# Optimization experiments

Measured on AMD Instinct MI355X. Metric: run time of the kernel, lower is better.

Reference implementation:

```python
import jax, jax.numpy as jnp
import numpy as np

H, Dh, D = 12, 64, 8          # heads, head dim, depth slices
DS = Dh // D                   # per-depth slice dim = 8
EPS = 1e-6
MAW_STRENGTH = 0.15
ALPHA = 1.0 + 10.0 * MAW_STRENGTH  # 2.5


def _min_max_norm(v, eps=1e-12):
    vmin = v.min(axis=-1, keepdims=True)
    vmax = v.max(axis=-1, keepdims=True)
    return (v - vmin) / jnp.maximum(vmax - vmin, eps)


def setup_inputs() -> dict:
    key = jax.random.key(0)
    ks = jax.random.split(key, 8)
    B, L, E = 2, 768, H * Dh
    s = 0.02
    return {
        "hidden_states": jax.random.normal(ks[0], (B, L, E), jnp.float32),
        "attention_mask": jnp.zeros((B, L), jnp.float32),  # additive mask
        "Wq": jax.random.normal(ks[1], (E, E), jnp.float32) * s,
        "bq": jnp.zeros((E,), jnp.float32),
        "Wk": jax.random.normal(ks[2], (E, E), jnp.float32) * s,
        "bk": jnp.zeros((E,), jnp.float32),
        "Wv": jax.random.normal(ks[3], (E, E), jnp.float32) * s,
        "bv": jnp.zeros((E,), jnp.float32),
    }


def reference(hidden_states, attention_mask, Wq, bq, Wk, bk, Wv, bv):
    B, L, E = hidden_states.shape
    # projections -> [B, H, L, Dh]
    q = (hidden_states @ Wq + bq).reshape(B, L, H, Dh).transpose(0, 2, 1, 3)
    k = (hidden_states @ Wk + bk).reshape(B, L, H, Dh).transpose(0, 2, 1, 3)
    v = (hidden_states @ Wv + bv).reshape(B, L, H, Dh).transpose(0, 2, 1, 3)

    # depth-wise expansion: split head dim into D slices of size DS
    qd = q.reshape(B, H, L, D, DS)
    kd = k.reshape(B, H, L, D, DS)
    scores = jnp.einsum("bhqds,bhkds->bhdqk", qd, kd) / jnp.sqrt(jnp.float32(DS))
    # additive mask [B, Lk] -> [B, 1, 1, 1, Lk]
    scores = scores + attention_mask[:, None, None, None, :]
    attn = jax.nn.softmax(scores, axis=-1)  # [B, H, D, Lq, Lk]

    # statistical depth gating (mode='stat')
    var_k = jnp.var(attn, axis=-1, ddof=1).mean(axis=(1, 3))          # [B, D]
    max_k = attn.max(axis=-1).mean(axis=(1, 3))                        # [B, D]
    p = jnp.clip(attn, EPS, None)
    ent = (-p * jnp.log(p)).sum(axis=-1).mean(axis=(1, 3))             # [B, D]
    hhi = (attn * attn).sum(axis=-1).mean(axis=(1, 3))                 # [B, D]

    score = (0.5 * _min_max_norm(var_k) + 0.3 * _min_max_norm(max_k)
             + 0.2 * _min_max_norm(hhi) - 0.4 * _min_max_norm(ent))
    weights = jax.nn.softmax(ALPHA * score, axis=-1)                   # [B, D]

    # depth compression -> [B, H, Lq, Lk]
    attn4 = jnp.einsum("bhdqk,bd->bhqk", attn, weights)
    ctx = jnp.einsum("bhqk,bhkd->bhqd", attn4, v)                      # [B, H, L, Dh]
    ctx = ctx.transpose(0, 2, 1, 3).reshape(B, L, H * Dh)
    return ctx, attn4
```

## Files before the change

kernel.cpp:

```cpp
#include <hip/hip_runtime.h>

#define BATCH 2
#define L_SEQ 768
#define NH 12
#define DH 64
#define ND 8
#define EMB 768
#define RSQRT8 0.35355339059327373f

#define OFF_Q    0
#define OFF_K    1179648
#define OFF_V    2359296
#define OFF_L    3538944
#define OFF_PART 3686400
#define OFF_P2   6045696
#define OFF_W    6046464

__global__ __launch_bounds__(256) void k1_qkv(
    const float* __restrict__ hs,
    const float* __restrict__ Wq, const float* __restrict__ bq,
    const float* __restrict__ Wk, const float* __restrict__ bk,
    const float* __restrict__ Wv, const float* __restrict__ bvp,
    float* __restrict__ qw, float* __restrict__ kw, float* __restrict__ vw)
{
    __shared__ float AsT[64][68];
    __shared__ float Bs[64][68];
    const int tid = threadIdx.x;
    const int tx = tid & 15, ty = tid >> 4;
    const int bx = blockIdx.x, by = blockIdx.y, gz = blockIdx.z;
    const float* W    = (gz == 0) ? Wq : (gz == 1 ? Wk : Wv);
    const float* bias = (gz == 0) ? bq : (gz == 1 ? bk : bvp);
    float* dst        = (gz == 0) ? qw : (gz == 1 ? kw : vw);

    const int ldc = tx * 4;

    float acc[4][4];
#pragma unroll
    for (int i = 0; i < 4; i++)
#pragma unroll
        for (int j = 0; j < 4; j++) acc[i][j] = 0.f;

    for (int k0 = 0; k0 < EMB; k0 += 64) {
        __syncthreads();
#pragma unroll
        for (int i = 0; i < 4; i++) {
            int r = ty + 16 * i;
            float4 a = *(const float4*)&hs[(size_t)(by * 64 + r) * EMB + k0 + ldc];
            AsT[ldc + 0][r] = a.x; AsT[ldc + 1][r] = a.y;
            AsT[ldc + 2][r] = a.z; AsT[ldc + 3][r] = a.w;
            *(float4*)&Bs[r][ldc] =
                *(const float4*)&W[(size_t)(k0 + r) * EMB + bx * 64 + ldc];
        }
        __syncthreads();
#pragma unroll 8
        for (int kk = 0; kk < 64; kk++) {
            float av[4], bb[4];
            *(float4*)av = *(const float4*)&AsT[kk][ty * 4];
            *(float4*)bb = *(const float4*)&Bs[kk][tx * 4];
#pragma unroll
            for (int i = 0; i < 4; i++)
#pragma unroll
                for (int j = 0; j < 4; j++)
                    acc[i][j] = fmaf(av[i], bb[j], acc[i][j]);
        }
    }

#pragma unroll
    for (int i = 0; i < 4; i++) {
        int m = by * 64 + ty * 4 + i;
        int b2 = m / L_SEQ, l = m % L_SEQ;
        float o[4];
#pragma unroll
        for (int j = 0; j < 4; j++) o[j] = acc[i][j] + bias[bx * 64 + tx * 4 + j];
        *(float4*)&dst[((size_t)(b2 * NH + bx) * L_SEQ + l) * DH + tx * 4] = *(float4*)o;
    }
}

__global__ __launch_bounds__(256) void k2_stats(
    const float* __restrict__ qw, const float* __restrict__ kw,
    const float* __restrict__ mask, float* __restrict__ part)
{
    __shared__ float k_lds[64 * 64];
    __shared__ float m_lds[64];
    const int tid = threadIdx.x;
    const int lane = tid & 63, w = tid >> 6;
    const int qr = lane >> 3, d = lane & 7;
    const int blk = blockIdx.x;
    const int kq = blk & 3;
    const int t2 = blk >> 2;
    const int bh = t2 / 12;
    const int q0 = (t2 % 12) * 64;
    const int b = bh / NH;
    const int qw0 = q0 + w * 16;

    float qf[2][8];
#pragma unroll
    for (int qq = 0; qq < 2; qq++) {
        const float* qp = &qw[((size_t)bh * L_SEQ + qw0 + qr + qq * 8) * DH + d * 8];
        *(float4*)&qf[qq][0] = *(const float4*)qp;
        *(float4*)&qf[qq][4] = *(const float4*)(qp + 4);
    }
    float S[2] = {0.f, 0.f}, T2[2] = {0.f, 0.f}, SL[2] = {0.f, 0.f};
    float M[2] = {-1e30f, -1e30f};

    const int kb0 = kq * 192;
    for (int c = 0; c < 3; c++) {
        const int kb = kb0 + c * 64;
        __syncthreads();
        {
            const float* src = &kw[((size_t)bh * L_SEQ + kb) * DH];
#pragma unroll
            for (int i = 0; i < 4; i++) {
                int f = tid + 256 * i;
                *(float4*)&k_lds[f * 4] = *(const float4*)&src[f * 4];
            }
            if (tid < 64) m_lds[tid] = mask[b * L_SEQ + kb + tid];
        }
        __syncthreads();
#pragma unroll 4
        for (int kk = 0; kk < 64; kk++) {
            float kv[8];
            *(float4*)&kv[0] = *(const float4*)&k_lds[kk * 64 + d * 8];
            *(float4*)&kv[4] = *(const float4*)&k_lds[kk * 64 + d * 8 + 4];
            float mval = m_lds[kk];
#pragma unroll
            for (int qq = 0; qq < 2; qq++) {
                float s = 0.f;
#pragma unroll
                for (int t = 0; t < 8; t++) s = fmaf(qf[qq][t], kv[t], s);
                s = fmaf(s, RSQRT8, mval);
                float e = __expf(s);
                S[qq] += e;
                T2[qq] = fmaf(e, e, T2[qq]);
                SL[qq] = fmaf(s, e, SL[qq]);
                M[qq] = fmaxf(M[qq], s);
            }
        }
    }
#pragma unroll
    for (int qq = 0; qq < 2; qq++) {
        int q = qw0 + qr + qq * 8;
        size_t base = (size_t)(bh * 8 + d) * 16;
        part[(base + 0 + kq) * 768 + q] = S[qq];
        part[(base + 4 + kq) * 768 + q] = T2[qq];
        part[(base + 8 + kq) * 768 + q] = SL[qq];
        part[(base + 12 + kq) * 768 + q] = M[qq];
    }
}

__global__ __launch_bounds__(256) void k3_reduce(
    const float* __restrict__ part, float* __restrict__ l_arr,
    float* __restrict__ part2)
{
    const int bdh = blockIdx.x;
    const int bd = bdh / 12, h = bdh % 12;
    const int b = bd >> 3, d = bd & 7;
    const int bh = b * NH + h;
    const int tid = threadIdx.x;
    const int lane = tid & 63, wave = tid >> 6;
    const size_t base = (size_t)(bh * 8 + d) * 16;
    float acc[4] = {0.f, 0.f, 0.f, 0.f};

    for (int q = tid; q < 768; q += 256) {
        float Sv = 0.f, T2v = 0.f, SLv = 0.f, Mv = -1e30f;
#pragma unroll
        for (int kq = 0; kq < 4; kq++) {
            Sv  += part[(base + 0 + kq) * 768 + q];
            T2v += part[(base + 4 + kq) * 768 + q];
            SLv += part[(base + 8 + kq) * 768 + q];
            Mv = fmaxf(Mv, part[(base + 12 + kq) * 768 + q]);
        }
        l_arr[(size_t)(bh * 8 + d) * 768 + q] = Sv;
        float inv = 1.0f / Sv;
        float hhi = T2v * inv * inv;
        float maxp = __expf(Mv) * inv;
        float ent = __logf(Sv) - SLv * inv;
        float var = (hhi - (1.0f / 768.0f)) * (1.0f / 767.0f);
        acc[0] += var; acc[1] += maxp; acc[2] += ent; acc[3] += hhi;
    }
    __shared__ float red[4][4];
#pragma unroll
    for (int st = 0; st < 4; st++) {
        float a = acc[st];
#pragma unroll
        for (int off = 32; off > 0; off >>= 1) a += __shfl_xor(a, off, 64);
        acc[st] = a;
    }
    if (lane == 0) {
#pragma unroll
        for (int st = 0; st < 4; st++) red[wave][st] = acc[st];
    }
    __syncthreads();
    if (tid == 0) {
#pragma unroll
        for (int st = 0; st < 4; st++)
            part2[(size_t)(bd * 12 + h) * 4 + st] =
                red[0][st] + red[1][st] + red[2][st] + red[3][st];
    }
}

__global__ __launch_bounds__(64) void k3_weights(
    const float* __restrict__ part2, float* __restrict__ wgt)
{
    __shared__ float stats_l[64];
    const int tid = threadIdx.x;
    {
        const int bd = tid >> 2, st = tid & 3;
        float s = 0.f;
#pragma unroll
        for (int h = 0; h < 12; h++) s += part2[(size_t)(bd * 12 + h) * 4 + st];
        stats_l[tid] = s * (1.0f / 9216.0f);
    }
    __syncthreads();
    if (tid == 0) {
        for (int b = 0; b < BATCH; b++) {
            float v[4][8];
            for (int st = 0; st < 4; st++)
                for (int d = 0; d < 8; d++) v[st][d] = stats_l[(b * 8 + d) * 4 + st];
            float nrm[4][8];
            for (int st = 0; st < 4; st++) {
                float mn = v[st][0], mx = v[st][0];
                for (int d = 1; d < 8; d++) { mn = fminf(mn, v[st][d]); mx = fmaxf(mx, v[st][d]); }
                float rng = fmaxf(mx - mn, 1e-12f);
                for (int d = 0; d < 8; d++) nrm[st][d] = (v[st][d] - mn) / rng;
            }
            float sc[8];
            for (int d = 0; d < 8; d++)
                sc[d] = 0.5f * nrm[0][d] + 0.3f * nrm[1][d] + 0.2f * nrm[3][d] - 0.4f * nrm[2][d];
            float m = 2.5f * sc[0];
            for (int d = 1; d < 8; d++) m = fmaxf(m, 2.5f * sc[d]);
            float e8[8]; float ssum = 0.f;
            for (int d = 0; d < 8; d++) { e8[d] = __expf(2.5f * sc[d] - m); ssum += e8[d]; }
            for (int d = 0; d < 8; d++) wgt[b * ND + d] = e8[d] / ssum;
        }
    }
}

__global__ __launch_bounds__(256) void k4_attn(
    const float* __restrict__ qw, const float* __restrict__ kw,
    const float* __restrict__ mask,
    const float* __restrict__ l_arr, const float* __restrict__ wgt,
    float* __restrict__ out_a4)
{
    __shared__ float k_lds[32 * 64];
    __shared__ float a4_lds[4][16 * 36];
    __shared__ float m_lds[32];
    const int tid = threadIdx.x;
    const int lane = tid & 63, w = tid >> 6;
    const int qr = lane >> 3, d = lane & 7;
    const int blk = blockIdx.x;
    const int kq = blk & 3;
    const int t2 = blk >> 2;
    const int bh = t2 / 12;
    const int q0 = (t2 % 12) * 64;
    const int b = bh / NH;
    const int qw0 = q0 + w * 16;

    float qf[2][8];
    float c0[2];
#pragma unroll
    for (int qq = 0; qq < 2; qq++) {
        int row = qw0 + qr + qq * 8;
        const float* qp = &qw[((size_t)bh * L_SEQ + row) * DH + d * 8];
        *(float4*)&qf[qq][0] = *(const float4*)qp;
        *(float4*)&qf[qq][4] = *(const float4*)(qp + 4);
        c0[qq] = wgt[b * ND + d] / l_arr[(size_t)(bh * 8 + d) * 768 + row];
    }

    const int kb0 = kq * 192;
    for (int c = 0; c < 6; c++) {
        const int kb = kb0 + c * 32;
        __syncthreads();
        {
            const float* ksrc = &kw[((size_t)bh * L_SEQ + kb) * DH];
#pragma unroll
            for (int i = 0; i < 2; i++) {
                int f = tid + 256 * i;
                *(float4*)&k_lds[f * 4] = *(const float4*)&ksrc[f * 4];
            }
            if (tid < 32) m_lds[tid] = mask[b * L_SEQ + kb + tid];
        }
        __syncthreads();

#pragma unroll
        for (int kk2 = 0; kk2 < 32; kk2 += 2) {
            float a4v[2][2];
#pragma unroll
            for (int u = 0; u < 2; u++) {
                int kk = kk2 + u;
                float kv[8];
                *(float4*)&kv[0] = *(const float4*)&k_lds[kk * 64 + d * 8];
                *(float4*)&kv[4] = *(const float4*)&k_lds[kk * 64 + d * 8 + 4];
                float mval = m_lds[kk];
#pragma unroll
                for (int qq = 0; qq < 2; qq++) {
                    float s = 0.f;
#pragma unroll
                    for (int t = 0; t < 8; t++) s = fmaf(qf[qq][t], kv[t], s);
                    s = fmaf(s, RSQRT8, mval);
                    a4v[u][qq] = c0[qq] * __expf(s);
                }
            }
#pragma unroll
            for (int u = 0; u < 2; u++)
#pragma unroll
                for (int qq = 0; qq < 2; qq++) {
                    float a = a4v[u][qq];
                    a += __shfl_xor(a, 1, 64);
                    a += __shfl_xor(a, 2, 64);
                    a += __shfl_xor(a, 4, 64);
                    a4v[u][qq] = a;
                }
#pragma unroll
            for (int u = 0; u < 2; u++) {
                int kk = kk2 + u;
                if (d < 2)
                    a4_lds[w][(qr + d * 8) * 36 + kk] = (d == 0) ? a4v[u][0] : a4v[u][1];
            }
        }
#pragma unroll
        for (int i = 0; i < 2; i++) {
            int f = lane + 64 * i;
            int row = f >> 3, c4 = (f & 7) * 4;
            *(float4*)&out_a4[((size_t)bh * L_SEQ + qw0 + row) * L_SEQ + kb + c4] =
                *(float4*)&a4_lds[w][row * 36 + c4];
        }
    }
}

__global__ __launch_bounds__(256) void k5_ctx(
    const float* __restrict__ vw, const float* __restrict__ out_a4,
    float* __restrict__ out_ctx)
{
    __shared__ float a4_lds[32 * 68];
    __shared__ float v_lds[64 * 64];
    const int tid = threadIdx.x;
    const int lane = tid & 63, w = tid >> 6;
    const int ty = (lane >> 4);
    const int tx = lane & 15;
    const int rbase = w * 8 + ty * 2;
    const int blk = blockIdx.x;
    const int bh = blk / 24;
    const int q0 = (blk % 24) * 32;
    const int b = bh / NH, h = bh % NH;

    const float* a4src = &out_a4[((size_t)bh * L_SEQ + q0) * L_SEQ];

    float acc[2][4];
#pragma unroll
    for (int qq = 0; qq < 2; qq++)
#pragma unroll
        for (int j = 0; j < 4; j++) acc[qq][j] = 0.f;

    for (int c = 0; c < 12; c++) {
        const int kb = c * 64;
        __syncthreads();
        {
#pragma unroll
            for (int i = 0; i < 2; i++) {
                int f = tid + 256 * i;
                int row = f >> 4, col = (f & 15) * 4;
                *(float4*)&a4_lds[row * 68 + col] =
                    *(const float4*)&a4src[(size_t)row * L_SEQ + kb + col];
            }
            const float* vsrc = &vw[((size_t)bh * L_SEQ + kb) * DH];
#pragma unroll
            for (int i = 0; i < 4; i++) {
                int f = tid + 256 * i;
                *(float4*)&v_lds[f * 4] = *(const float4*)&vsrc[f * 4];
            }
        }
        __syncthreads();
#pragma unroll
        for (int kk4 = 0; kk4 < 16; kk4++) {
            float af[2][4];
            *(float4*)&af[0][0] = *(const float4*)&a4_lds[(rbase + 0) * 68 + kk4 * 4];
            *(float4*)&af[1][0] = *(const float4*)&a4_lds[(rbase + 1) * 68 + kk4 * 4];
#pragma unroll
            for (int u = 0; u < 4; u++) {
                float4 vv = *(const float4*)&v_lds[(kk4 * 4 + u) * 64 + tx * 4];
#pragma unroll
                for (int qq = 0; qq < 2; qq++) {
                    acc[qq][0] = fmaf(af[qq][u], vv.x, acc[qq][0]);
                    acc[qq][1] = fmaf(af[qq][u], vv.y, acc[qq][1]);
                    acc[qq][2] = fmaf(af[qq][u], vv.z, acc[qq][2]);
                    acc[qq][3] = fmaf(af[qq][u], vv.w, acc[qq][3]);
                }
            }
        }
    }
#pragma unroll
    for (int qq = 0; qq < 2; qq++)
        *(float4*)&out_ctx[((size_t)b * L_SEQ + q0 + rbase + qq) * EMB + h * DH + tx * 4] =
            *(float4*)&acc[qq][0];
}

extern "C" void kernel_launch(void* const* d_in, const int* in_sizes, int n_in,
                              void* d_out, int out_size, void* d_ws, size_t ws_size,
                              hipStream_t stream)
{
    const float* hs   = (const float*)d_in[0];
    const float* mask = (const float*)d_in[1];
    const float* Wq   = (const float*)d_in[2];
    const float* bq   = (const float*)d_in[3];
    const float* Wk   = (const float*)d_in[4];
    const float* bk   = (const float*)d_in[5];
    const float* Wv   = (const float*)d_in[6];
    const float* bv   = (const float*)d_in[7];

    float* ws = (float*)d_ws;
    float* qw = ws + OFF_Q;
    float* kw = ws + OFF_K;
    float* vw = ws + OFF_V;
    float* l_arr = ws + OFF_L;
    float* part  = ws + OFF_PART;
    float* part2 = ws + OFF_P2;
    float* wgt   = ws + OFF_W;

    float* out_ctx = (float*)d_out;
    float* out_a4  = (float*)d_out + (size_t)BATCH * L_SEQ * EMB;

    k1_qkv<<<dim3(12, 24, 3), 256, 0, stream>>>(hs, Wq, bq, Wk, bk, Wv, bv, qw, kw, vw);
    k2_stats<<<dim3(1152), 256, 0, stream>>>(qw, kw, mask, part);
    k3_reduce<<<dim3(192), 256, 0, stream>>>(part, l_arr, part2);
    k3_weights<<<dim3(1), 64, 0, stream>>>(part2, wgt);
    k4_attn<<<dim3(1152), 256, 0, stream>>>(qw, kw, mask, l_arr, wgt, out_a4);
    k5_ctx<<<dim3(576), 256, 0, stream>>>(vw, out_a4, out_ctx);
}
```

Before: 361.9 us.

## Fuse depth-compressed attention and context kernels into one pass

Merges the attention-probability kernel and the context matmul so each block computes a 32-row tile of attn4, writes it out, and multiplies it by V straight from shared memory. This avoids re-reading the large attn4 tensor from global memory and removes one launch. Each thread now owns a full query row (64 q values in registers) and loops over all 8 depths, replacing the cross-lane shuffle reduction. The trade-offs are higher register pressure and half as many blocks (576 vs 1152), which may lower occupancy.

Result: faster. 331.4 us (-8.4%).

```diff
diff --git a/kernel.cpp b/kernel.cpp
--- a/kernel.cpp
+++ b/kernel.cpp
@@ -236,163 +236,114 @@
     }
 }
 
-__global__ __launch_bounds__(256) void k4_attn(
+__global__ __launch_bounds__(256) void k45_fused(
     const float* __restrict__ qw, const float* __restrict__ kw,
-    const float* __restrict__ mask,
+    const float* __restrict__ vw, const float* __restrict__ mask,
     const float* __restrict__ l_arr, const float* __restrict__ wgt,
-    float* __restrict__ out_a4)
-{
-    __shared__ float k_lds[32 * 64];
-    __shared__ float a4_lds[4][16 * 36];
-    __shared__ float m_lds[32];
+    float* __restrict__ out_a4, float* __restrict__ out_ctx)
+{
+    __shared__ float k_lds[64 * 68];
+    __shared__ float v_lds[64 * 64];
+    __shared__ float a4_lds[4][8 * 68];
+    __shared__ float m_lds[64];
+
     const int tid = threadIdx.x;
     const int lane = tid & 63, w = tid >> 6;
-    const int qr = lane >> 3, d = lane & 7;
-    const int blk = blockIdx.x;
-    const int kq = blk & 3;
-    const int t2 = blk >> 2;
-    const int bh = t2 / 12;
-    const int q0 = (t2 % 12) * 64;
-    const int b = bh / NH;
-    const int qw0 = q0 + w * 16;
-
-    float qf[2][8];
-    float c0[2];
-#pragma unroll
-    for (int qq = 0; qq < 2; qq++) {
-        int row = qw0 + qr + qq * 8;
-        const float* qp = &qw[((size_t)bh * L_SEQ + row) * DH + d * 8];
-        *(float4*)&qf[qq][0] = *(const float4*)qp;
-        *(float4*)&qf[qq][4] = *(const float4*)(qp + 4);
-        c0[qq] = wgt[b * ND + d] / l_arr[(size_t)(bh * 8 + d) * 768 + row];
-    }
-
-    const int kb0 = kq * 192;
-    for (int c = 0; c < 6; c++) {
-        const int kb = kb0 + c * 32;
-        __syncthreads();
-        {
-            const float* ksrc = &kw[((size_t)bh * L_SEQ + kb) * DH];
-#pragma unroll
-            for (int i = 0; i < 2; i++) {
-                int f = tid + 256 * i;
-                *(float4*)&k_lds[f * 4] = *(const float4*)&ksrc[f * 4];
-            }
-            if (tid < 32) m_lds[tid] = mask[b * L_SEQ + kb + tid];
-        }
-        __syncthreads();
-
-#pragma unroll
-        for (int kk2 = 0; kk2 < 32; kk2 += 2) {
-            float a4v[2][2];
-#pragma unroll
-            for (int u = 0; u < 2; u++) {
-                int kk = kk2 + u;
-                float kv[8];
-                *(float4*)&kv[0] = *(const float4*)&k_lds[kk * 64 + d * 8];
-                *(float4*)&kv[4] = *(const float4*)&k_lds[kk * 64 + d * 8 + 4];
-                float mval = m_lds[kk];
-#pragma unroll
-                for (int qq = 0; qq < 2; qq++) {
-                    float s = 0.f;
-#pragma unroll
-                    for (int t = 0; t < 8; t++) s = fmaf(qf[qq][t], kv[t], s);
-                    s = fmaf(s, RSQRT8, mval);
-                    a4v[u][qq] = c0[qq] * __expf(s);
-                }
-            }
-#pragma unroll
-            for (int u = 0; u < 2; u++)
-#pragma unroll
-                for (int qq = 0; qq < 2; qq++) {
-                    float a = a4v[u][qq];
-                    a += __shfl_xor(a, 1, 64);
-                    a += __shfl_xor(a, 2, 64);
-                    a += __shfl_xor(a, 4, 64);
-                    a4v[u][qq] = a;
-                }
-#pragma unroll
-            for (int u = 0; u < 2; u++) {
-                int kk = kk2 + u;
-                if (d < 2)
-                    a4_lds[w][(qr + d * 8) * 36 + kk] = (d == 0) ? a4v[u][0] : a4v[u][1];
-            }
-        }
-#pragma unroll
-        for (int i = 0; i < 2; i++) {
-            int f = lane + 64 * i;
-            int row = f >> 3, c4 = (f & 7) * 4;
-            *(float4*)&out_a4[((size_t)bh * L_SEQ + qw0 + row) * L_SEQ + kb + c4] =
-                *(float4*)&a4_lds[w][row * 36 + c4];
-        }
-    }
-}
-
-__global__ __launch_bounds__(256) void k5_ctx(
-    const float* __restrict__ vw, const float* __restrict__ out_a4,
-    float* __restrict__ out_ctx)
-{
-    __shared__ float a4_lds[32 * 68];
-    __shared__ float v_lds[64 * 64];
-    const int tid = threadIdx.x;
-    const int lane = tid & 63, w = tid >> 6;
-    const int ty = (lane >> 4);
-    const int tx = lane & 15;
-    const int rbase = w * 8 + ty * 2;
     const int blk = blockIdx.x;
     const int bh = blk / 24;
     const int q0 = (blk % 24) * 32;
     const int b = bh / NH, h = bh % NH;
-
-    const float* a4src = &out_a4[((size_t)bh * L_SEQ + q0) * L_SEQ];
-
-    float acc[2][4];
-#pragma unroll
-    for (int qq = 0; qq < 2; qq++)
-#pragma unroll
-        for (int j = 0; j < 4; j++) acc[qq][j] = 0.f;
+    const int qw0 = q0 + w * 8;
+
+    const int qr = lane >> 3;
+    const int kc = lane & 7;
+    const int rb = lane >> 4;
+    const int cb = lane & 15;
+
+    float qf[64];
+    {
+        const float* qp = &qw[((size_t)bh * L_SEQ + qw0 + qr) * DH];
+#pragma unroll
+        for (int t = 0; t < 16; t++)
+            *(float4*)&qf[t * 4] = *(const float4*)&qp[t * 4];
+    }
+    float c0[8];
+#pragma unroll
+    for (int d = 0; d < 8; d++)
+        c0[d] = wgt[b * ND + d] / l_arr[(size_t)(bh * 8 + d) * L_SEQ + qw0 + qr];
+
+    float4 acc0 = {0.f, 0.f, 0.f, 0.f};
+    float4 acc1 = {0.f, 0.f, 0.f, 0.f};
 
     for (int c = 0; c < 12; c++) {
         const int kb = c * 64;
         __syncthreads();
         {
-#pragma unroll
-            for (int i = 0; i < 2; i++) {
+            const float* ksrc = &kw[((size_t)bh * L_SEQ + kb) * DH];
+            const float* vsrc = &vw[((size_t)bh * L_SEQ + kb) * DH];
+#pragma unroll
+            for (int i = 0; i < 4; i++) {
                 int f = tid + 256 * i;
                 int row = f >> 4, col = (f & 15) * 4;
-                *(float4*)&a4_lds[row * 68 + col] =
-                    *(const float4*)&a4src[(size_t)row * L_SEQ + kb + col];
-            }
-            const float* vsrc = &vw[((size_t)bh * L_SEQ + kb) * DH];
-#pragma unroll
-            for (int i = 0; i < 4; i++) {
-                int f = tid + 256 * i;
+                *(float4*)&k_lds[row * 68 + col] = *(const float4*)&ksrc[f * 4];
                 *(float4*)&v_lds[f * 4] = *(const float4*)&vsrc[f * 4];
             }
-        }
-        __syncthreads();
-#pragma unroll
-        for (int kk4 = 0; kk4 < 16; kk4++) {
-            float af[2][4];
-            *(float4*)&af[0][0] = *(const float4*)&a4_lds[(rbase + 0) * 68 + kk4 * 4];
-            *(float4*)&af[1][0] = *(const float4*)&a4_lds[(rbase + 1) * 68 + kk4 * 4];
+            if (tid < 64) m_lds[tid] = mask[b * L_SEQ + kb + tid];
+        }
+        __syncthreads();
+
+#pragma unroll 2
+        for (int j = 0; j < 8; j++) {
+            const int k = kc + 8 * j;
+            const float* krow = &k_lds[k * 68];
+            const float mval = m_lds[k];
+            float a4 = 0.f;
+#pragma unroll
+            for (int d = 0; d < 8; d++) {
+                float kv[8];
+                *(float4*)&kv[0] = *(const float4*)&krow[d * 8];
+                *(float4*)&kv[4] = *(const float4*)&krow[d * 8 + 4];
+                float s = 0.f;
+#pragma unroll
+                for (int t = 0; t < 8; t++) s = fmaf(qf[d * 8 + t], kv[t], s);
+                s = fmaf(s, RSQRT8, mval);
+                a4 = fmaf(c0[d], __expf(s), a4);
+            }
+            a4_lds[w][qr * 68 + k] = a4;
+        }
+
+        {
+            const int r = lane >> 3, c8 = (lane & 7) * 8;
+            float* dst = &out_a4[((size_t)bh * L_SEQ + qw0 + r) * L_SEQ + kb + c8];
+            *(float4*)&dst[0] = *(const float4*)&a4_lds[w][r * 68 + c8];
+            *(float4*)&dst[4] = *(const float4*)&a4_lds[w][r * 68 + c8 + 4];
+        }
+
+#pragma unroll 4
+        for (int kg = 0; kg < 16; kg++) {
+            float a0[4], a1[4];
+            *(float4*)a0 = *(const float4*)&a4_lds[w][rb * 68 + kg * 4];
+            *(float4*)a1 = *(const float4*)&a4_lds[w][(rb + 4) * 68 + kg * 4];
 #pragma unroll
             for (int u = 0; u < 4; u++) {
-                float4 vv = *(const float4*)&v_lds[(kk4 * 4 + u) * 64 + tx * 4];
-#pragma unroll
-                for (int qq = 0; qq < 2; qq++) {
-                    acc[qq][0] = fmaf(af[qq][u], vv.x, acc[qq][0]);
-                    acc[qq][1] = fmaf(af[qq][u], vv.y, acc[qq][1]);
-                    acc[qq][2] = fmaf(af[qq][u], vv.z, acc[qq][2]);
-                    acc[qq][3] = fmaf(af[qq][u], vv.w, acc[qq][3]);
-                }
-            }
-        }
-    }
-#pragma unroll
-    for (int qq = 0; qq < 2; qq++)
-        *(float4*)&out_ctx[((size_t)b * L_SEQ + q0 + rbase + qq) * EMB + h * DH + tx * 4] =
-            *(float4*)&acc[qq][0];
+                float4 vv = *(const float4*)&v_lds[(kg * 4 + u) * 64 + cb * 4];
+                acc0.x = fmaf(a0[u], vv.x, acc0.x);
+                acc0.y = fmaf(a0[u], vv.y, acc0.y);
+                acc0.z = fmaf(a0[u], vv.z, acc0.z);
+                acc0.w = fmaf(a0[u], vv.w, acc0.w);
+                acc1.x = fmaf(a1[u], vv.x, acc1.x);
+                acc1.y = fmaf(a1[u], vv.y, acc1.y);
+                acc1.z = fmaf(a1[u], vv.z, acc1.z);
+                acc1.w = fmaf(a1[u], vv.w, acc1.w);
+            }
+        }
+    }
+
+    {
+        const int row0 = qw0 + rb, row1 = qw0 + rb + 4;
+        *(float4*)&out_ctx[((size_t)b * L_SEQ + row0) * EMB + h * DH + cb * 4] = acc0;
+        *(float4*)&out_ctx[((size_t)b * L_SEQ + row1) * EMB + h * DH + cb * 4] = acc1;
+    }
 }
 
 extern "C" void kernel_launch(void* const* d_in, const int* in_sizes, int n_in,
@@ -424,6 +375,5 @@
     k2_stats<<<dim3(1152), 256, 0, stream>>>(qw, kw, mask, part);
     k3_reduce<<<dim3(192), 256, 0, stream>>>(part, l_arr, part2);
     k3_weights<<<dim3(1), 64, 0, stream>>>(part2, wgt);
-    k4_attn<<<dim3(1152), 256, 0, stream>>>(qw, kw, mask, l_arr, wgt, out_a4);
-    k5_ctx<<<dim3(576), 256, 0, stream>>>(vw, out_a4, out_ctx);
-}
+    k45_fused<<<dim3(576), 256, 0, stream>>>(qw, kw, vw, mask, l_arr, wgt, out_a4, out_ctx);
+}
```
